# Performance work log

Measured on AMD Instinct MI355X. Metric: run time of the kernel, lower is better.

## Reference

```python
import jax, jax.numpy as jnp
import numpy as np

USER_COUNT = 100000
ITEM_COUNT = 50000
LATENT = 64
N_LAYERS = 3
NEG_SLOPE = 0.2


def _xavier(key, shape):
    fan_in, fan_out = shape[-2], shape[-1]
    lim = jnp.sqrt(6.0 / (fan_in + fan_out))
    return jax.random.uniform(key, shape, jnp.float32, -lim, lim)


def setup_inputs() -> dict:
    key = jax.random.key(0)
    ks = jax.random.split(key, 20)
    E = 2400000
    edge_index = jax.random.randint(ks[0], (2, E), 0, USER_COUNT + ITEM_COUNT, dtype=jnp.int64)
    user = jax.random.randint(ks[1], (4096,), 0, USER_COUNT, dtype=jnp.int64)
    item = jax.random.randint(ks[2], (4096,), 0, ITEM_COUNT, dtype=jnp.int64)
    inp = {"user": user, "item": item, "edge_index": edge_index}
    # online encoder params
    inp["user_emb_o"] = _xavier(ks[3], (USER_COUNT, LATENT))
    inp["item_emb_o"] = _xavier(ks[4], (ITEM_COUNT, LATENT))
    inp["W_o"] = _xavier(ks[5], (N_LAYERS, LATENT, LATENT))
    inp["att_src_o"] = _xavier(ks[6], (N_LAYERS, 1, LATENT))[:, 0, :]
    inp["att_dst_o"] = _xavier(ks[7], (N_LAYERS, 1, LATENT))[:, 0, :]
    inp["bias_o"] = jnp.zeros((N_LAYERS, LATENT), jnp.float32)
    # target encoder params (momentum copy; frozen in torch)
    inp["user_emb_t"] = _xavier(ks[8], (USER_COUNT, LATENT))
    inp["item_emb_t"] = _xavier(ks[9], (ITEM_COUNT, LATENT))
    inp["W_t"] = _xavier(ks[10], (N_LAYERS, LATENT, LATENT))
    inp["att_src_t"] = _xavier(ks[11], (N_LAYERS, 1, LATENT))[:, 0, :]
    inp["att_dst_t"] = _xavier(ks[12], (N_LAYERS, 1, LATENT))[:, 0, :]
    inp["bias_t"] = jnp.zeros((N_LAYERS, LATENT), jnp.float32)
    # predictor Linear(latent, latent)
    inp["pred_W"] = _xavier(ks[13], (LATENT, LATENT))
    inp["pred_b"] = jnp.zeros((LATENT,), jnp.float32)
    return inp


def _gat_conv(x, src, dst, n_nodes, W, a_src, a_dst, b):
    # PyG GATConv, heads=1, concat=True, add_self_loops handled by caller.
    h = x @ W                                   # [N, F]
    e = jax.nn.leaky_relu(jnp.take(h @ a_src, src) + jnp.take(h @ a_dst, dst), NEG_SLOPE)  # [E]
    m = jax.ops.segment_max(e, dst, num_segments=n_nodes)
    m = jnp.where(jnp.isfinite(m), m, 0.0)
    ex = jnp.exp(e - jnp.take(m, dst))
    den = jax.ops.segment_sum(ex, dst, num_segments=n_nodes)
    alpha = ex / jnp.take(den, dst)             # softmax over incoming edges per dst
    msg = alpha[:, None] * jnp.take(h, src, axis=0)  # [E, F]
    return jax.ops.segment_sum(msg, dst, num_segments=n_nodes) + b


def _encode(user_emb, item_emb, W, a_src, a_dst, bias, src, dst):
    x = jnp.concatenate([user_emb, item_emb], axis=0)  # [N, F]
    n_nodes = x.shape[0]
    for l in range(N_LAYERS):
        x = _gat_conv(x, src, dst, n_nodes, W[l], a_src[l], a_dst[l], bias[l])
    return x[:user_emb.shape[0]], x[user_emb.shape[0]:]


def reference(user_emb_o, item_emb_o, W_o, att_src_o, att_dst_o, bias_o,
              user_emb_t, item_emb_t, W_t, att_src_t, att_dst_t, bias_t,
              pred_W, pred_b, user, item, edge_index):
    n_nodes = user_emb_o.shape[0] + item_emb_o.shape[0]
    loops = jnp.arange(n_nodes, dtype=edge_index.dtype)
    src = jnp.concatenate([edge_index[0], loops])  # add self loops (PyG default)
    dst = jnp.concatenate([edge_index[1], loops])
    u_all_o, i_all_o = _encode(user_emb_o, item_emb_o, W_o, att_src_o, att_dst_o, bias_o, src, dst)
    u_all_t, i_all_t = _encode(user_emb_t, item_emb_t, W_t, att_src_t, att_dst_t, bias_t, src, dst)
    u_online = jnp.take(u_all_o, user, axis=0)
    i_online = jnp.take(i_all_o, item, axis=0)
    u_target = jnp.take(u_all_t, user, axis=0)
    i_target = jnp.take(i_all_t, item, axis=0)
    return (u_online @ pred_W.T + pred_b, u_target, i_online @ pred_W.T + pred_b, i_target)
```

## Files before the change

### kernel.cpp

```cpp
#include <hip/hip_runtime.h>
#include <math.h>
#include <stdint.h>

#define LAT 64
#define SLICE 16384
#define BIN_CHUNK 1024

static inline int cdiv(int a, int b) { return (a + b - 1) / b; }

__global__ void k_scan1(const int* __restrict__ cnt, int N, int* __restrict__ out, int* __restrict__ blk_sums) {
    __shared__ int sdata[256];
    int t = threadIdx.x, b = blockIdx.x;
    int base = b * 1024 + t * 4;
    int v[4];
    int s = 0;
#pragma unroll
    for (int u = 0; u < 4; u++) { int i = base + u; v[u] = (i < N) ? cnt[i] : 0; s += v[u]; }
    sdata[t] = s; __syncthreads();
    for (int off = 1; off < 256; off <<= 1) {
        int x = (t >= off) ? sdata[t - off] : 0;
        __syncthreads();
        sdata[t] += x;
        __syncthreads();
    }
    int run = sdata[t] - s;
#pragma unroll
    for (int u = 0; u < 4; u++) { int i = base + u; if (i < N) out[i] = run; run += v[u]; }
    if (t == 255) blk_sums[b] = sdata[255];
}

__global__ void k_scan2(int* __restrict__ blk_sums, int NB) {
    __shared__ int sdata[256];
    int t = threadIdx.x;
    int v = (t < NB) ? blk_sums[t] : 0;
    sdata[t] = v; __syncthreads();
    for (int off = 1; off < 256; off <<= 1) {
        int x = (t >= off) ? sdata[t - off] : 0;
        __syncthreads();
        sdata[t] += x;
        __syncthreads();
    }
    if (t < NB) blk_sums[t] = sdata[t] - v;
}

__global__ void k_scan3(int* __restrict__ row_ptr, const int* __restrict__ blk_offs, int N, int ET) {
    int t = threadIdx.x, b = blockIdx.x;
    int base = b * 1024 + t * 4;
    int off = blk_offs[b];
#pragma unroll
    for (int u = 0; u < 4; u++) { int i = base + u; if (i < N) row_ptr[i] += off; }
    if (b == 0 && t == 0) row_ptr[N] = ET;
}

__global__ __launch_bounds__(256) void k_binA(const int* __restrict__ src_arr, const int* __restrict__ dst_arr,
                                              int E, int N, int ET, int rsz, int bcap,
                                              int2* __restrict__ buckets, int* __restrict__ gcur,
                                              int* __restrict__ cnt) {
    __shared__ int lcnt[8], lbase[8];
    int t = threadIdx.x;
    for (int base = blockIdx.x * BIN_CHUNK; base < ET; base += gridDim.x * BIN_CHUNK) {
        if (t < 8) lcnt[t] = 0;
        __syncthreads();
        int s[4], d[4], r[4], lofs[4];
        int nval = 0;
        if (base + BIN_CHUNK <= E) {
            int4 s4 = ((const int4*)(src_arr + base))[t];
            int4 d4 = ((const int4*)(dst_arr + base))[t];
            s[0] = s4.x; s[1] = s4.y; s[2] = s4.z; s[3] = s4.w;
            d[0] = d4.x; d[1] = d4.y; d[2] = d4.z; d[3] = d4.w;
            nval = 4;
        } else {
            for (int k = 0; k < 4; k++) {
                int e = base + t * 4 + k;
                if (e < ET) {
                    if (e < E) { s[nval] = src_arr[e]; d[nval] = dst_arr[e]; }
                    else { s[nval] = e - E; d[nval] = e - E; }
                    nval++;
                }
            }
        }
        for (int k = 0; k < nval; k++) {
            r[k] = d[k] / rsz;
            lofs[k] = atomicAdd(&lcnt[r[k]], 1);
            atomicAdd(&cnt[d[k]], 1);
        }
        __syncthreads();
        if (t < 8) lbase[t] = atomicAdd(&gcur[t], lcnt[t]);
        __syncthreads();
        for (int k = 0; k < nval; k++) {
            buckets[(size_t)r[k] * bcap + lbase[r[k]] + lofs[k]] = make_int2(s[k], d[k]);
        }
        __syncthreads();
    }
}

__global__ __launch_bounds__(256) void k_binB(const int2* __restrict__ buckets, int bcap,
                                              const int* __restrict__ gcur,
                                              const int* __restrict__ row_ptr, int* __restrict__ cnt,
                                              int* __restrict__ csr_src) {
    int r = blockIdx.x & 7;
    int nb = blockIdx.x >> 3;
    int stride = (gridDim.x >> 3) * 256;
    int total = gcur[r];
    const int* bp = (const int*)(buckets + (size_t)r * bcap);
    for (int i = nb * 256 + threadIdx.x; i < total; i += stride) {
        int s = __builtin_nontemporal_load(bp + 2 * i);
        int d = __builtin_nontemporal_load(bp + 2 * i + 1);
        int pos = atomicAdd(&cnt[d], 1);
        csr_src[row_ptr[d] + pos] = s;
    }
}

__global__ void k_count(const int* __restrict__ dst_arr, int E, int N, int* __restrict__ cnt) {
    int e = blockIdx.x * blockDim.x + threadIdx.x;
    int ET = E + N;
    if (e < ET) {
        int d = (e < E) ? dst_arr[e] : (e - E);
        atomicAdd(&cnt[d], 1);
    }
}

__global__ void k_scatter(const int* __restrict__ src_arr, const int* __restrict__ dst_arr, int E, int N,
                          const int* __restrict__ row_ptr, int* __restrict__ cnt, int* __restrict__ csr_src) {
    int ET = E + N;
    int slice = blockIdx.x >> 3;
    int range = blockIdx.x & 7;
    int rsz = (N + 7) >> 3;
    int lo = range * rsz;
    int hi = lo + rsz; if (hi > N) hi = N;
    int base = slice * SLICE;
    int end = base + SLICE; if (end > ET) end = ET;
    for (int e = base + threadIdx.x; e < end; e += 256) {
        int s, d;
        if (e < E) { s = src_arr[e]; d = dst_arr[e]; }
        else { s = e - E; d = e - E; }
        if (d >= lo && d < hi) {
            int pos = atomicAdd(&cnt[d], 1);
            csr_src[row_ptr[d] + pos] = s;
        }
    }
}

__global__ __launch_bounds__(256) void k_gemm2m(const float* __restrict__ xo, const float* __restrict__ xt,
        const float* __restrict__ ueo, const float* __restrict__ ieo,
        const float* __restrict__ uet, const float* __restrict__ iet, int NU,
        const float* __restrict__ Wo, const float* __restrict__ Wt,
        const float* __restrict__ atso, const float* __restrict__ atdo,
        const float* __restrict__ atst, const float* __restrict__ atdt,
        float* __restrict__ h2, float* __restrict__ asp, float* __restrict__ adp, int N) {
    __shared__ float sW[64 * 64];
    __shared__ float sX[128 * 65];
    __shared__ float sAs[64], sAd[64];
    int enc = blockIdx.x & 1;
    int bb = blockIdx.x >> 1;
    const float* x = enc ? xt : xo;
    const float* ue = enc ? uet : ueo;
    const float* ie = enc ? iet : ieo;
    const float* W = enc ? Wt : Wo;
    const float* att_s = enc ? atst : atso;
    const float* att_d = enc ? atdt : atdo;
    float* h2e = h2 + enc * 64;
    int t = threadIdx.x;
    int row0 = bb * 128;
    {
        const float4* Wv = (const float4*)W;
        float4* sWv = (float4*)sW;
#pragma unroll
        for (int u = 0; u < 4; u++) sWv[t + 256 * u] = Wv[t + 256 * u];
    }
    if (t < 64) { sAs[t] = att_s[t]; sAd[t] = att_d[t]; }
    {
#pragma unroll
        for (int u = 0; u < 8; u++) {
            int idx = t + 256 * u;
            int r = idx >> 4, c4 = idx & 15;
            int grow = row0 + r;
            float4 v = make_float4(0.f, 0.f, 0.f, 0.f);
            if (grow < N) {
                const float* base = x ? (x + (size_t)grow * 64)
                                      : (grow < NU ? ue + (size_t)grow * 64 : ie + (size_t)(grow - NU) * 64);
                v = ((const float4*)base)[c4];
            }
            int cc = c4 * 4;
            sX[r * 65 + cc] = v.x; sX[r * 65 + cc + 1] = v.y; sX[r * 65 + cc + 2] = v.z; sX[r * 65 + cc + 3] = v.w;
        }
    }
    __syncthreads();
    int rl = t >> 2;
    int g = t & 3;
    int c0 = g * 16;
    int rA = rl * 2, rB = rA + 1;
    float accA[16], accB[16];
#pragma unroll
    for (int j = 0; j < 16; j++) { accA[j] = 0.f; accB[j] = 0.f; }
    for (int k = 0; k < 64; k++) {
        float xa = sX[rA * 65 + k];
        float xb = sX[rB * 65 + k];
        const float4* wr = (const float4*)&sW[k * 64 + c0];
        float4 w0 = wr[0], w1 = wr[1], w2 = wr[2], w3 = wr[3];
        accA[0] += xa * w0.x; accA[1] += xa * w0.y; accA[2] += xa * w0.z; accA[3] += xa * w0.w;
        accA[4] += xa * w1.x; accA[5] += xa * w1.y; accA[6] += xa * w1.z; accA[7] += xa * w1.w;
        accA[8] += xa * w2.x; accA[9] += xa * w2.y; accA[10] += xa * w2.z; accA[11] += xa * w2.w;
        accA[12] += xa * w3.x; accA[13] += xa * w3.y; accA[14] += xa * w3.z; accA[15] += xa * w3.w;
        accB[0] += xb * w0.x; accB[1] += xb * w0.y; accB[2] += xb * w0.z; accB[3] += xb * w0.w;
        accB[4] += xb * w1.x; accB[5] += xb * w1.y; accB[6] += xb * w1.z; accB[7] += xb * w1.w;
        accB[8] += xb * w2.x; accB[9] += xb * w2.y; accB[10] += xb * w2.z; accB[11] += xb * w2.w;
        accB[12] += xb * w3.x; accB[13] += xb * w3.y; accB[14] += xb * w3.z; accB[15] += xb * w3.w;
    }
    float sA = 0.f, dA = 0.f, sB = 0.f, dB = 0.f;
#pragma unroll
    for (int j = 0; j < 16; j++) {
        sA += accA[j] * sAs[c0 + j]; dA += accA[j] * sAd[c0 + j];
        sB += accB[j] * sAs[c0 + j]; dB += accB[j] * sAd[c0 + j];
    }
    sA += __shfl_xor(sA, 1); sA += __shfl_xor(sA, 2);
    dA += __shfl_xor(dA, 1); dA += __shfl_xor(dA, 2);
    sB += __shfl_xor(sB, 1); sB += __shfl_xor(sB, 2);
    dB += __shfl_xor(dB, 1); dB += __shfl_xor(dB, 2);
    int rowA = row0 + rA, rowB = row0 + rB;
    if (rowA < N) {
        if (g == 0) { asp[(size_t)rowA * 2 + enc] = sA; adp[(size_t)rowA * 2 + enc] = dA; }
        float4* hv = (float4*)&h2e[(size_t)rowA * 128 + c0];
        hv[0] = make_float4(accA[0], accA[1], accA[2], accA[3]);
        hv[1] = make_float4(accA[4], accA[5], accA[6], accA[7]);
        hv[2] = make_float4(accA[8], accA[9], accA[10], accA[11]);
        hv[3] = make_float4(accA[12], accA[13], accA[14], accA[15]);
    }
    if (rowB < N) {
        if (g == 0) { asp[(size_t)rowB * 2 + enc] = sB; adp[(size_t)rowB * 2 + enc] = dB; }
        float4* hv = (float4*)&h2e[(size_t)rowB * 128 + c0];
        hv[0] = make_float4(accB[0], accB[1], accB[2], accB[3]);
        hv[1] = make_float4(accB[4], accB[5], accB[6], accB[7]);
        hv[2] = make_float4(accB[8], accB[9], accB[10], accB[11]);
        hv[3] = make_float4(accB[12], accB[13], accB[14], accB[15]);
    }
}

__global__ __launch_bounds__(256) void k_agg2(const float* __restrict__ h2,
                                              const int* __restrict__ row_ptr, const int* __restrict__ csr_src,
                                              const float2* __restrict__ asv, const float2* __restrict__ adv,
                                              const float* __restrict__ bias_o, const float* __restrict__ bias_t,
                                              float* __restrict__ xo, float* __restrict__ xt, int N,
                                              const int* __restrict__ selu, const int* __restrict__ seli,
                                              int nSel, int nSelU, int NU,
                                              float* __restrict__ selxo, float* __restrict__ outT_u,
                                              float* __restrict__ outT_i) {
    int wid = threadIdx.x >> 6, lane = threadIdx.x & 63;
    int r = blockIdx.x * 4 + wid;
    int d;
    float *po, *pt;
    if (selu) {
        if (r >= nSel) return;
        if (r < nSelU) { d = selu[r]; pt = outT_u + (size_t)r * 64; }
        else { int rr = r - nSelU; d = seli[rr] + NU; pt = outT_i + (size_t)rr * 64; }
        po = selxo + (size_t)r * 64;
    } else {
        if (r >= N) return;
        d = r;
        po = xo + (size_t)d * 64;
        pt = xt + (size_t)d * 64;
    }
    int s0 = row_ptr[d], s1 = row_ptr[d + 1];
    float2 advv = adv[d];
    int j0 = s0 + lane;
    int sv0 = 0; float eo0 = -1e30f, et0 = -1e30f;
    if (j0 < s1) {
        sv0 = csr_src[j0];
        float2 a2 = asv[sv0];
        float eo = a2.x + advv.x; eo0 = (eo > 0.f) ? eo : 0.2f * eo;
        float et = a2.y + advv.y; et0 = (et > 0.f) ? et : 0.2f * et;
    }
    float mo = eo0, mt = et0;
    for (int j = j0 + 64; j < s1; j += 64) {
        float2 a2 = asv[csr_src[j]];
        float eo = a2.x + advv.x; eo = (eo > 0.f) ? eo : 0.2f * eo; mo = fmaxf(mo, eo);
        float et = a2.y + advv.y; et = (et > 0.f) ? et : 0.2f * et; mt = fmaxf(mt, et);
    }
#pragma unroll
    for (int o = 32; o; o >>= 1) { mo = fmaxf(mo, __shfl_xor(mo, o)); mt = fmaxf(mt, __shfl_xor(mt, o)); }
    float exo0 = (j0 < s1) ? expf(eo0 - mo) : 0.f;
    float ext0 = (j0 < s1) ? expf(et0 - mt) : 0.f;
    float so = exo0, st = ext0;
    for (int j = j0 + 64; j < s1; j += 64) {
        float2 a2 = asv[csr_src[j]];
        float eo = a2.x + advv.x; eo = (eo > 0.f) ? eo : 0.2f * eo; so += expf(eo - mo);
        float et = a2.y + advv.y; et = (et > 0.f) ? et : 0.2f * et; st += expf(et - mt);
    }
#pragma unroll
    for (int o = 32; o; o >>= 1) { so += __shfl_xor(so, o); st += __shfl_xor(st, o); }
    float invo = 1.f / so, invt = 1.f / st;
    exo0 *= invo; ext0 *= invt;
    int sub = lane >> 4, c4 = lane & 15;
    float4 ao = make_float4(0.f, 0.f, 0.f, 0.f);
    float4 at4 = make_float4(0.f, 0.f, 0.f, 0.f);
    for (int cb = s0; cb < s1; cb += 64) {
        int sv; float wo, wt;
        if (cb == s0) { sv = sv0; wo = exo0; wt = ext0; }
        else {
            int jj = cb + lane; sv = 0; wo = 0.f; wt = 0.f;
            if (jj < s1) {
                sv = csr_src[jj];
                float2 a2 = asv[sv];
                float eo = a2.x + advv.x; eo = (eo > 0.f) ? eo : 0.2f * eo; wo = expf(eo - mo) * invo;
                float et = a2.y + advv.y; et = (et > 0.f) ? et : 0.2f * et; wt = expf(et - mt) * invt;
            }
        }
        int c = s1 - cb; if (c > 64) c = 64;
        int q = 0;
        for (; q + 8 <= c; q += 8) {
            int ilA = q + sub, ilB = q + 4 + sub;
            int sA = __shfl(sv, ilA), sB = __shfl(sv, ilB);
            float oA = __shfl(wo, ilA), oB = __shfl(wo, ilB);
            float tA = __shfl(wt, ilA), tB = __shfl(wt, ilB);
            const float* ha = h2 + (size_t)sA * 128 + (c4 << 2);
            const float* hb = h2 + (size_t)sB * 128 + (c4 << 2);
            float4 hoA = *(const float4*)ha;
            float4 htA = *(const float4*)(ha + 64);
            float4 hoB = *(const float4*)hb;
            float4 htB = *(const float4*)(hb + 64);
            ao.x += oA * hoA.x; ao.y += oA * hoA.y; ao.z += oA * hoA.z; ao.w += oA * hoA.w;
            at4.x += tA * htA.x; at4.y += tA * htA.y; at4.z += tA * htA.z; at4.w += tA * htA.w;
            ao.x += oB * hoB.x; ao.y += oB * hoB.y; ao.z += oB * hoB.z; ao.w += oB * hoB.w;
            at4.x += tB * htB.x; at4.y += tB * htB.y; at4.z += tB * htB.z; at4.w += tB * htB.w;
        }
        for (; q < c; q += 4) {
            int il = q + sub;
            int s = __shfl(sv, il);
            float o_ = __shfl(wo, il);
            float t_ = __shfl(wt, il);
            const float* hb = h2 + (size_t)s * 128 + (c4 << 2);
            float4 ho = *(const float4*)hb;
            float4 ht = *(const float4*)(hb + 64);
            ao.x += o_ * ho.x; ao.y += o_ * ho.y; ao.z += o_ * ho.z; ao.w += o_ * ho.w;
            at4.x += t_ * ht.x; at4.y += t_ * ht.y; at4.z += t_ * ht.z; at4.w += t_ * ht.w;
        }
    }
#pragma unroll
    for (int o = 16; o <= 32; o <<= 1) {
        ao.x += __shfl_xor(ao.x, o); ao.y += __shfl_xor(ao.y, o);
        ao.z += __shfl_xor(ao.z, o); ao.w += __shfl_xor(ao.w, o);
        at4.x += __shfl_xor(at4.x, o); at4.y += __shfl_xor(at4.y, o);
        at4.z += __shfl_xor(at4.z, o); at4.w += __shfl_xor(at4.w, o);
    }
    if (lane < 16) {
        float4 bo = ((const float4*)bias_o)[c4];
        ao.x += bo.x; ao.y += bo.y; ao.z += bo.z; ao.w += bo.w;
        ((float4*)po)[c4] = ao;
        float4 bt = ((const float4*)bias_t)[c4];
        at4.x += bt.x; at4.y += bt.y; at4.z += bt.z; at4.w += bt.w;
        ((float4*)pt)[c4] = at4;
    }
}

__global__ __launch_bounds__(256) void k_gemm(const float* __restrict__ x,
                                              const float* __restrict__ ue, const float* __restrict__ ie, int NU,
                                              const float* __restrict__ W,
                                              const float* __restrict__ att_s, const float* __restrict__ att_d,
                                              float* __restrict__ h, float* __restrict__ as_, float* __restrict__ ad_,
                                              int N) {
    __shared__ float sW[64 * 64];
    __shared__ float sX[128 * 65];
    __shared__ float sAs[64], sAd[64];
    int t = threadIdx.x;
    int row0 = blockIdx.x * 128;
    {
        const float4* Wv = (const float4*)W;
        float4* sWv = (float4*)sW;
#pragma unroll
        for (int u = 0; u < 4; u++) sWv[t + 256 * u] = Wv[t + 256 * u];
    }
    if (t < 64) { sAs[t] = att_s[t]; sAd[t] = att_d[t]; }
    {
#pragma unroll
        for (int u = 0; u < 8; u++) {
            int idx = t + 256 * u;
            int r = idx >> 4, c4 = idx & 15;
            int grow = row0 + r;
            float4 v = make_float4(0.f, 0.f, 0.f, 0.f);
            if (grow < N) {
                const float* base = x ? (x + (size_t)grow * 64)
                                      : (grow < NU ? ue + (size_t)grow * 64 : ie + (size_t)(grow - NU) * 64);
                v = ((const float4*)base)[c4];
            }
            int cc = c4 * 4;
            sX[r * 65 + cc] = v.x; sX[r * 65 + cc + 1] = v.y; sX[r * 65 + cc + 2] = v.z; sX[r * 65 + cc + 3] = v.w;
        }
    }
    __syncthreads();
    int rl = t >> 2;
    int g = t & 3;
    int c0 = g * 16;
    int rA = rl * 2, rB = rA + 1;
    float accA[16], accB[16];
#pragma unroll
    for (int j = 0; j < 16; j++) { accA[j] = 0.f; accB[j] = 0.f; }
    for (int k = 0; k < 64; k++) {
        float xa = sX[rA * 65 + k];
        float xb = sX[rB * 65 + k];
        const float4* wr = (const float4*)&sW[k * 64 + c0];
        float4 w0 = wr[0], w1 = wr[1], w2 = wr[2], w3 = wr[3];
        accA[0] += xa * w0.x; accA[1] += xa * w0.y; accA[2] += xa * w0.z; accA[3] += xa * w0.w;
        accA[4] += xa * w1.x; accA[5] += xa * w1.y; accA[6] += xa * w1.z; accA[7] += xa * w1.w;
        accA[8] += xa * w2.x; accA[9] += xa * w2.y; accA[10] += xa * w2.z; accA[11] += xa * w2.w;
        accA[12] += xa * w3.x; accA[13] += xa * w3.y; accA[14] += xa * w3.z; accA[15] += xa * w3.w;
        accB[0] += xb * w0.x; accB[1] += xb * w0.y; accB[2] += xb * w0.z; accB[3] += xb * w0.w;
        accB[4] += xb * w1.x; accB[5] += xb * w1.y; accB[6] += xb * w1.z; accB[7] += xb * w1.w;
        accB[8] += xb * w2.x; accB[9] += xb * w2.y; accB[10] += xb * w2.z; accB[11] += xb * w2.w;
        accB[12] += xb * w3.x; accB[13] += xb * w3.y; accB[14] += xb * w3.z; accB[15] += xb * w3.w;
    }
    float sA = 0.f, dA = 0.f, sB = 0.f, dB = 0.f;
#pragma unroll
    for (int j = 0; j < 16; j++) {
        sA += accA[j] * sAs[c0 + j]; dA += accA[j] * sAd[c0 + j];
        sB += accB[j] * sAs[c0 + j]; dB += accB[j] * sAd[c0 + j];
    }
    sA += __shfl_xor(sA, 1); sA += __shfl_xor(sA, 2);
    dA += __shfl_xor(dA, 1); dA += __shfl_xor(dA, 2);
    sB += __shfl_xor(sB, 1); sB += __shfl_xor(sB, 2);
    dB += __shfl_xor(dB, 1); dB += __shfl_xor(dB, 2);
    int rowA = row0 + rA, rowB = row0 + rB;
    if (rowA < N) {
        if (g == 0) { as_[rowA] = sA; ad_[rowA] = dA; }
        float4* hv = (float4*)&h[(size_t)rowA * 64 + c0];
        hv[0] = make_float4(accA[0], accA[1], accA[2], accA[3]);
        hv[1] = make_float4(accA[4], accA[5], accA[6], accA[7]);
        hv[2] = make_float4(accA[8], accA[9], accA[10], accA[11]);
        hv[3] = make_float4(accA[12], accA[13], accA[14], accA[15]);
    }
    if (rowB < N) {
        if (g == 0) { as_[rowB] = sB; ad_[rowB] = dB; }
        float4* hv = (float4*)&h[(size_t)rowB * 64 + c0];
        hv[0] = make_float4(accB[0], accB[1], accB[2], accB[3]);
        hv[1] = make_float4(accB[4], accB[5], accB[6], accB[7]);
        hv[2] = make_float4(accB[8], accB[9], accB[10], accB[11]);
        hv[3] = make_float4(accB[12], accB[13], accB[14], accB[15]);
    }
}

__global__ __launch_bounds__(256) void k_agg(const float* __restrict__ h,
                                             const int* __restrict__ row_ptr, const int* __restrict__ csr_src,
                                             const float* __restrict__ as_, const float* __restrict__ ad_,
                                             const float* __restrict__ bias, float* __restrict__ xout, int N) {
    int wid = threadIdx.x >> 6, lane = threadIdx.x & 63;
    int d = blockIdx.x * 4 + wid;
    if (d >= N) return;
    int s0 = row_ptr[d], s1 = row_ptr[d + 1];
    float adv = ad_[d];
    int j0 = s0 + lane;
    int sv0 = 0; float ev0 = -1e30f;
    if (j0 < s1) {
        sv0 = csr_src[j0];
        float e = as_[sv0] + adv;
        ev0 = (e > 0.f) ? e : 0.2f * e;
    }
    float m = ev0;
    for (int j = j0 + 64; j < s1; j += 64) {
        float e = as_[csr_src[j]] + adv;
        e = (e > 0.f) ? e : 0.2f * e;
        m = fmaxf(m, e);
    }
#pragma unroll
    for (int o = 32; o; o >>= 1) m = fmaxf(m, __shfl_xor(m, o));
    float ex0 = (j0 < s1) ? expf(ev0 - m) : 0.f;
    float sum = ex0;
    for (int j = j0 + 64; j < s1; j += 64) {
        float e = as_[csr_src[j]] + adv;
        e = (e > 0.f) ? e : 0.2f * e;
        sum += expf(e - m);
    }
#pragma unroll
    for (int o = 32; o; o >>= 1) sum += __shfl_xor(sum, o);
    float inv = 1.f / sum;
    ex0 *= inv;
    int sub = lane >> 4;
    int c4 = lane & 15;
    float4 acc = make_float4(0.f, 0.f, 0.f, 0.f);
    for (int cbase = s0; cbase < s1; cbase += 64) {
        int sv; float ex;
        if (cbase == s0) { sv = sv0; ex = ex0; }
        else {
            int jj = cbase + lane;
            sv = 0; ex = 0.f;
            if (jj < s1) {
                sv = csr_src[jj];
                float e = as_[sv] + adv;
                e = (e > 0.f) ? e : 0.2f * e;
                ex = expf(e - m) * inv;
            }
        }
        int cnt2 = s1 - cbase; if (cnt2 > 64) cnt2 = 64;
        for (int q = 0; q < cnt2; q += 4) {
            int il = q + sub;
            float w = __shfl(ex, il);
            int s = __shfl(sv, il);
            const float4 hv = *(const float4*)&h[(size_t)s * 64 + (c4 << 2)];
            acc.x += w * hv.x; acc.y += w * hv.y; acc.z += w * hv.z; acc.w += w * hv.w;
        }
    }
#pragma unroll
    for (int o = 16; o <= 32; o <<= 1) {
        acc.x += __shfl_xor(acc.x, o);
        acc.y += __shfl_xor(acc.y, o);
        acc.z += __shfl_xor(acc.z, o);
        acc.w += __shfl_xor(acc.w, o);
    }
    if (lane < 16) {
        float4 bv = ((const float4*)bias)[c4];
        acc.x += bv.x; acc.y += bv.y; acc.z += bv.z; acc.w += bv.w;
        ((float4*)&xout[(size_t)d * 64])[c4] = acc;
    }
}

__global__ __launch_bounds__(256) void k_pred(const float* __restrict__ x, const int* __restrict__ idx,
                                              int nIdx, int rowOff, const float* __restrict__ W,
                                              const float* __restrict__ bvec, float* __restrict__ out) {
    __shared__ float sWt[64 * 65];
    int t = threadIdx.x;
#pragma unroll
    for (int u = 0; u < 16; u++) {
        int i = u * 256 + t;
        int c = i >> 6, k = i & 63;
        sWt[k * 65 + c] = W[i];
    }
    __syncthreads();
    int wid = t >> 6, lane = t & 63;
    int r = blockIdx.x * 4 + wid;
    if (r >= nIdx) return;
    int node = idx ? (idx[r] + rowOff) : (r + rowOff);
    float xr = x[(size_t)node * 64 + lane];
    float acc = bvec[lane];
    for (int k = 0; k < 64; k++)
        acc += __shfl(xr, k) * sWt[k * 65 + lane];
    out[(size_t)r * 64 + lane] = acc;
}

__global__ void k_gather(const float* __restrict__ x, const int* __restrict__ idx, int nIdx, int rowOff,
                         float* __restrict__ out) {
    int t = blockIdx.x * blockDim.x + threadIdx.x;
    if (t < nIdx * 64) {
        int r = t >> 6, c = t & 63;
        int node = idx[r] + rowOff;
        out[t] = x[(size_t)node * 64 + c];
    }
}

extern "C" void kernel_launch(void* const* d_in, const int* in_sizes, int n_in,
                              void* d_out, int out_size, void* d_ws, size_t ws_size,
                              hipStream_t stream) {
    const int* user = (const int*)d_in[0];
    const int* item = (const int*)d_in[1];
    const int* edge = (const int*)d_in[2];
    const float* user_emb_o = (const float*)d_in[3];
    const float* item_emb_o = (const float*)d_in[4];
    const float* W_o = (const float*)d_in[5];
    const float* att_src_o = (const float*)d_in[6];
    const float* att_dst_o = (const float*)d_in[7];
    const float* bias_o = (const float*)d_in[8];
    const float* user_emb_t = (const float*)d_in[9];
    const float* item_emb_t = (const float*)d_in[10];
    const float* W_t = (const float*)d_in[11];
    const float* att_src_t = (const float*)d_in[12];
    const float* att_dst_t = (const float*)d_in[13];
    const float* bias_t = (const float*)d_in[14];
    const float* pred_W = (const float*)d_in[15];
    const float* pred_b = (const float*)d_in[16];
    float* out = (float*)d_out;

    int E = in_sizes[2] / 2;
    int NU = in_sizes[3] / LAT;
    int NI = in_sizes[4] / LAT;
    int N = NU + NI;
    int ET = E + N;
    int nU = in_sizes[0];
    int nI = in_sizes[1];
    int nSel = nU + nI;
    int rsz = (N + 7) >> 3;

    const int* src_arr = edge;
    const int* dst_arr = edge + E;

    auto al = [](size_t v) { return (v + 255) & ~(size_t)255; };

    char* p = (char*)d_ws;
    float* x_o   = (float*)p;  p += al((size_t)N * LAT * 4);
    float* x_t   = (float*)p;  p += al((size_t)N * LAT * 4);
    float* h2    = (float*)p;  p += al((size_t)N * 2 * LAT * 4);
    float* asv   = (float*)p;  p += al((size_t)N * 8);
    float* adv   = (float*)p;  p += al((size_t)N * 8);
    int* row_ptr = (int*)p;    p += al((size_t)(N + 1) * 4);
    int* cnt     = (int*)p;    p += al((size_t)N * 4);
    int* csr_src = (int*)p;    p += al((size_t)ET * 4);
    int* blk     = (int*)p;    p += al(4096);
    int* gcur    = (int*)p;    p += al(64);
    float* xsel  = (float*)p;  p += al((size_t)nSel * LAT * 4);
    size_t need_primary = (size_t)(p - (char*)d_ws);

    int bcap = ET / 8 + 16384;
    int2* buckets = (int2*)x_o;

    bool primary = ws_size >= need_primary;

    if (primary) {
        hipMemsetAsync(cnt, 0, (size_t)N * 4, stream);
        hipMemsetAsync(gcur, 0, 32, stream);
        k_binA<<<1024, 256, 0, stream>>>(src_arr, dst_arr, E, N, ET, rsz, bcap, buckets, gcur, cnt);
        int NB = cdiv(N, 1024);
        k_scan1<<<NB, 256, 0, stream>>>(cnt, N, row_ptr, blk);
        k_scan2<<<1, 256, 0, stream>>>(blk, NB);
        k_scan3<<<NB, 256, 0, stream>>>(row_ptr, blk, N, ET);
        hipMemsetAsync(cnt, 0, (size_t)N * 4, stream);
        k_binB<<<1024, 256, 0, stream>>>(buckets, bcap, gcur, row_ptr, cnt, csr_src);

        for (int l = 0; l < 3; l++) {
            const float* xo_in = (l == 0) ? nullptr : x_o;
            const float* xt_in = (l == 0) ? nullptr : x_t;
            k_gemm2m<<<cdiv(N, 128) * 2, 256, 0, stream>>>(xo_in, xt_in,
                    user_emb_o, item_emb_o, user_emb_t, item_emb_t, NU,
                    W_o + l * 4096, W_t + l * 4096,
                    att_src_o + l * 64, att_dst_o + l * 64,
                    att_src_t + l * 64, att_dst_t + l * 64,
                    h2, asv, adv, N);
            if (l < 2) {
                k_agg2<<<cdiv(N, 4), 256, 0, stream>>>(h2, row_ptr, csr_src,
                        (const float2*)asv, (const float2*)adv,
                        bias_o + l * 64, bias_t + l * 64,
                        x_o, x_t, N,
                        nullptr, nullptr, 0, 0, NU, nullptr, nullptr, nullptr);
            } else {
                k_agg2<<<cdiv(nSel, 4), 256, 0, stream>>>(h2, row_ptr, csr_src,
                        (const float2*)asv, (const float2*)adv,
                        bias_o + l * 64, bias_t + l * 64,
                        nullptr, nullptr, N,
                        user, item, nSel, nU, NU,
                        xsel, out + (size_t)nU * LAT, out + (size_t)3 * nU * LAT);
            }
        }
        k_pred<<<cdiv(nU, 4), 256, 0, stream>>>(xsel, nullptr, nU, 0, pred_W, pred_b, out);
        k_pred<<<cdiv(nI, 4), 256, 0, stream>>>(xsel, nullptr, nI, nU, pred_W, pred_b,
                                                out + (size_t)2 * nU * LAT);
        return;
    }

    p = (char*)d_ws;
    float* x_cur = (float*)p;  p += al((size_t)N * LAT * 4);
    float* h     = (float*)p;  p += al((size_t)N * LAT * 4);
    float* as_   = (float*)p;  p += al((size_t)N * 4);
    float* ad_   = (float*)p;  p += al((size_t)N * 4);
    row_ptr = (int*)p;         p += al((size_t)(N + 1) * 4);
    cnt     = (int*)p;         p += al((size_t)N * 4);
    csr_src = (int*)p;         p += al((size_t)ET * 4);
    blk     = (int*)p;         p += al(4096);

    hipMemsetAsync(cnt, 0, (size_t)N * 4, stream);
    k_count<<<cdiv(ET, 256), 256, 0, stream>>>(dst_arr, E, N, cnt);
    int NB = cdiv(N, 1024);
    k_scan1<<<NB, 256, 0, stream>>>(cnt, N, row_ptr, blk);
    k_scan2<<<1, 256, 0, stream>>>(blk, NB);
    k_scan3<<<NB, 256, 0, stream>>>(row_ptr, blk, N, ET);
    hipMemsetAsync(cnt, 0, (size_t)N * 4, stream);
    k_scatter<<<cdiv(ET, SLICE) * 8, 256, 0, stream>>>(src_arr, dst_arr, E, N, row_ptr, cnt, csr_src);

    auto run_encoder = [&](const float* ue, const float* ie, const float* Wl,
                           const float* asl, const float* adl, const float* bl) {
        for (int l = 0; l < 3; l++) {
            const float* xin = (l == 0) ? nullptr : x_cur;
            k_gemm<<<cdiv(N, 128), 256, 0, stream>>>(xin, ue, ie, NU, Wl + l * 64 * 64, asl + l * 64,
                                                     adl + l * 64, h, as_, ad_, N);
            k_agg<<<cdiv(N, 4), 256, 0, stream>>>(h, row_ptr, csr_src, as_, ad_, bl + l * 64, x_cur, N);
        }
    };

    run_encoder(user_emb_o, item_emb_o, W_o, att_src_o, att_dst_o, bias_o);
    k_pred<<<cdiv(nU, 4), 256, 0, stream>>>(x_cur, user, nU, 0, pred_W, pred_b, out);
    k_pred<<<cdiv(nI, 4), 256, 0, stream>>>(x_cur, item, nI, NU, pred_W, pred_b, out + (size_t)2 * nU * LAT);

    run_encoder(user_emb_t, item_emb_t, W_t, att_src_t, att_dst_t, bias_t);
    k_gather<<<cdiv(nU * LAT, 256), 256, 0, stream>>>(x_cur, user, nU, 0, out + (size_t)nU * LAT);
    k_gather<<<cdiv(nI * LAT, 256), 256, 0, stream>>>(x_cur, item, nI, NU, out + (size_t)3 * nU * LAT);
}
```

Baseline: 847.5 us.

## Build CSR from binned buckets with implicit self-loops and countdown placement

Self-loop edges are no longer materialized in the bucket pass. The scan adds one per node and writes each node's self-loop into the first CSR slot. Degree counting moves from random atomics in the streaming bin pass to a separate pass over the destination-sorted buckets, which should improve atomic locality. The scatter pass counts down from the counts instead of re-zeroing them, which removes one memset, and gcur is zeroed in the same memset. The two predictor launches are merged into one, at the cost of an extra read pass over the buckets.

Measured after the change: 875.9 us. 1.03x slower.

```diff
diff --git a/kernel.cpp b/kernel.cpp
--- a/kernel.cpp
+++ b/kernel.cpp
@@ -15,7 +15,7 @@
     int v[4];
     int s = 0;
 #pragma unroll
-    for (int u = 0; u < 4; u++) { int i = base + u; v[u] = (i < N) ? cnt[i] : 0; s += v[u]; }
+    for (int u = 0; u < 4; u++) { int i = base + u; v[u] = (i < N) ? (cnt[i] + 1) : 0; s += v[u]; }
     sdata[t] = s; __syncthreads();
     for (int off = 1; off < 256; off <<= 1) {
         int x = (t >= off) ? sdata[t - off] : 0;
@@ -43,22 +43,29 @@
     if (t < NB) blk_sums[t] = sdata[t] - v;
 }
 
-__global__ void k_scan3(int* __restrict__ row_ptr, const int* __restrict__ blk_offs, int N, int ET) {
+__global__ void k_scan3(int* __restrict__ row_ptr, const int* __restrict__ blk_offs, int N, int ET,
+                        int* __restrict__ csr_src) {
     int t = threadIdx.x, b = blockIdx.x;
     int base = b * 1024 + t * 4;
     int off = blk_offs[b];
 #pragma unroll
-    for (int u = 0; u < 4; u++) { int i = base + u; if (i < N) row_ptr[i] += off; }
+    for (int u = 0; u < 4; u++) {
+        int i = base + u;
+        if (i < N) {
+            int fin = row_ptr[i] + off;
+            row_ptr[i] = fin;
+            csr_src[fin] = i;
+        }
+    }
     if (b == 0 && t == 0) row_ptr[N] = ET;
 }
 
 __global__ __launch_bounds__(256) void k_binA(const int* __restrict__ src_arr, const int* __restrict__ dst_arr,
-                                              int E, int N, int ET, int rsz, int bcap,
-                                              int2* __restrict__ buckets, int* __restrict__ gcur,
-                                              int* __restrict__ cnt) {
+                                              int E, int rsz, int bcap,
+                                              int2* __restrict__ buckets, int* __restrict__ gcur) {
     __shared__ int lcnt[8], lbase[8];
     int t = threadIdx.x;
-    for (int base = blockIdx.x * BIN_CHUNK; base < ET; base += gridDim.x * BIN_CHUNK) {
+    for (int base = blockIdx.x * BIN_CHUNK; base < E; base += gridDim.x * BIN_CHUNK) {
         if (t < 8) lcnt[t] = 0;
         __syncthreads();
         int s[4], d[4], r[4], lofs[4];
@@ -72,17 +79,12 @@
         } else {
             for (int k = 0; k < 4; k++) {
                 int e = base + t * 4 + k;
-                if (e < ET) {
-                    if (e < E) { s[nval] = src_arr[e]; d[nval] = dst_arr[e]; }
-                    else { s[nval] = e - E; d[nval] = e - E; }
-                    nval++;
-                }
+                if (e < E) { s[nval] = src_arr[e]; d[nval] = dst_arr[e]; nval++; }
             }
         }
         for (int k = 0; k < nval; k++) {
             r[k] = d[k] / rsz;
             lofs[k] = atomicAdd(&lcnt[r[k]], 1);
-            atomicAdd(&cnt[d[k]], 1);
         }
         __syncthreads();
         if (t < 8) lbase[t] = atomicAdd(&gcur[t], lcnt[t]);
@@ -91,6 +93,19 @@
             buckets[(size_t)r[k] * bcap + lbase[r[k]] + lofs[k]] = make_int2(s[k], d[k]);
         }
         __syncthreads();
+    }
+}
+
+__global__ __launch_bounds__(256) void k_binCnt(const int2* __restrict__ buckets, int bcap,
+                                                const int* __restrict__ gcur, int* __restrict__ cnt) {
+    int r = blockIdx.x & 7;
+    int nb = blockIdx.x >> 3;
+    int stride = (gridDim.x >> 3) * 256;
+    int total = gcur[r];
+    const int* bp = (const int*)(buckets + (size_t)r * bcap);
+    for (int i = nb * 256 + threadIdx.x; i < total; i += stride) {
+        int d = __builtin_nontemporal_load(bp + 2 * i + 1);
+        atomicAdd(&cnt[d], 1);
     }
 }
 
@@ -106,7 +121,7 @@
     for (int i = nb * 256 + threadIdx.x; i < total; i += stride) {
         int s = __builtin_nontemporal_load(bp + 2 * i);
         int d = __builtin_nontemporal_load(bp + 2 * i + 1);
-        int pos = atomicAdd(&cnt[d], 1);
+        int pos = atomicSub(&cnt[d], 1);
         csr_src[row_ptr[d] + pos] = s;
     }
 }
@@ -118,6 +133,36 @@
         int d = (e < E) ? dst_arr[e] : (e - E);
         atomicAdd(&cnt[d], 1);
     }
+}
+
+__global__ void k_scan3f(int* __restrict__ row_ptr, const int* __restrict__ blk_offs, int N, int ET) {
+    int t = threadIdx.x, b = blockIdx.x;
+    int base = b * 1024 + t * 4;
+    int off = blk_offs[b];
+#pragma unroll
+    for (int u = 0; u < 4; u++) { int i = base + u; if (i < N) row_ptr[i] += off; }
+    if (b == 0 && t == 0) row_ptr[N] = ET;
+}
+
+__global__ void k_scan1f(const int* __restrict__ cnt, int N, int* __restrict__ out, int* __restrict__ blk_sums) {
+    __shared__ int sdata[256];
+    int t = threadIdx.x, b = blockIdx.x;
+    int base = b * 1024 + t * 4;
+    int v[4];
+    int s = 0;
+#pragma unroll
+    for (int u = 0; u < 4; u++) { int i = base + u; v[u] = (i < N) ? cnt[i] : 0; s += v[u]; }
+    sdata[t] = s; __syncthreads();
+    for (int off = 1; off < 256; off <<= 1) {
+        int x = (t >= off) ? sdata[t - off] : 0;
+        __syncthreads();
+        sdata[t] += x;
+        __syncthreads();
+    }
+    int run = sdata[t] - s;
+#pragma unroll
+    for (int u = 0; u < 4; u++) { int i = base + u; if (i < N) out[i] = run; run += v[u]; }
+    if (t == 255) blk_sums[b] = sdata[255];
 }
 
 __global__ void k_scatter(const int* __restrict__ src_arr, const int* __restrict__ dst_arr, int E, int N,
@@ -511,6 +556,29 @@
     }
 }
 
+__global__ __launch_bounds__(256) void k_pred2(const float* __restrict__ x, int nU, int nI,
+                                               const float* __restrict__ W, const float* __restrict__ bvec,
+                                               float* __restrict__ outU, float* __restrict__ outI) {
+    __shared__ float sWt[64 * 65];
+    int t = threadIdx.x;
+#pragma unroll
+    for (int u = 0; u < 16; u++) {
+        int i = u * 256 + t;
+        int c = i >> 6, k = i & 63;
+        sWt[k * 65 + c] = W[i];
+    }
+    __syncthreads();
+    int wid = t >> 6, lane = t & 63;
+    int r = blockIdx.x * 4 + wid;
+    if (r >= nU + nI) return;
+    float xr = x[(size_t)r * 64 + lane];
+    float acc = bvec[lane];
+    for (int k = 0; k < 64; k++)
+        acc += __shfl(xr, k) * sWt[k * 65 + lane];
+    float* dst = (r < nU) ? (outU + (size_t)r * 64) : (outI + (size_t)(r - nU) * 64);
+    dst[lane] = acc;
+}
+
 __global__ __launch_bounds__(256) void k_pred(const float* __restrict__ x, const int* __restrict__ idx,
                                               int nIdx, int rowOff, const float* __restrict__ W,
                                               const float* __restrict__ bvec, float* __restrict__ out) {
@@ -588,27 +656,26 @@
     float* asv   = (float*)p;  p += al((size_t)N * 8);
     float* adv   = (float*)p;  p += al((size_t)N * 8);
     int* row_ptr = (int*)p;    p += al((size_t)(N + 1) * 4);
-    int* cnt     = (int*)p;    p += al((size_t)N * 4);
+    int* cnt     = (int*)p;    size_t cntsz = al((size_t)N * 4); p += cntsz;
+    int* gcur    = (int*)p;    p += al(64);
     int* csr_src = (int*)p;    p += al((size_t)ET * 4);
     int* blk     = (int*)p;    p += al(4096);
-    int* gcur    = (int*)p;    p += al(64);
     float* xsel  = (float*)p;  p += al((size_t)nSel * LAT * 4);
     size_t need_primary = (size_t)(p - (char*)d_ws);
 
-    int bcap = ET / 8 + 16384;
+    int bcap = E / 8 + 16384;
     int2* buckets = (int2*)x_o;
 
     bool primary = ws_size >= need_primary;
 
     if (primary) {
-        hipMemsetAsync(cnt, 0, (size_t)N * 4, stream);
-        hipMemsetAsync(gcur, 0, 32, stream);
-        k_binA<<<1024, 256, 0, stream>>>(src_arr, dst_arr, E, N, ET, rsz, bcap, buckets, gcur, cnt);
+        hipMemsetAsync(cnt, 0, cntsz + 64, stream);
+        k_binA<<<1024, 256, 0, stream>>>(src_arr, dst_arr, E, rsz, bcap, buckets, gcur);
+        k_binCnt<<<128, 256, 0, stream>>>(buckets, bcap, gcur, cnt);
         int NB = cdiv(N, 1024);
         k_scan1<<<NB, 256, 0, stream>>>(cnt, N, row_ptr, blk);
         k_scan2<<<1, 256, 0, stream>>>(blk, NB);
-        k_scan3<<<NB, 256, 0, stream>>>(row_ptr, blk, N, ET);
-        hipMemsetAsync(cnt, 0, (size_t)N * 4, stream);
+        k_scan3<<<NB, 256, 0, stream>>>(row_ptr, blk, N, ET, csr_src);
         k_binB<<<1024, 256, 0, stream>>>(buckets, bcap, gcur, row_ptr, cnt, csr_src);
 
         for (int l = 0; l < 3; l++) {
@@ -635,9 +702,8 @@
                         xsel, out + (size_t)nU * LAT, out + (size_t)3 * nU * LAT);
             }
         }
-        k_pred<<<cdiv(nU, 4), 256, 0, stream>>>(xsel, nullptr, nU, 0, pred_W, pred_b, out);
-        k_pred<<<cdiv(nI, 4), 256, 0, stream>>>(xsel, nullptr, nI, nU, pred_W, pred_b,
-                                                out + (size_t)2 * nU * LAT);
+        k_pred2<<<cdiv(nSel, 4), 256, 0, stream>>>(xsel, nU, nI, pred_W, pred_b,
+                                                   out, out + (size_t)2 * nU * LAT);
         return;
     }
 
@@ -654,9 +720,9 @@
     hipMemsetAsync(cnt, 0, (size_t)N * 4, stream);
     k_count<<<cdiv(ET, 256), 256, 0, stream>>>(dst_arr, E, N, cnt);
     int NB = cdiv(N, 1024);
-    k_scan1<<<NB, 256, 0, stream>>>(cnt, N, row_ptr, blk);
+    k_scan1f<<<NB, 256, 0, stream>>>(cnt, N, row_ptr, blk);
     k_scan2<<<1, 256, 0, stream>>>(blk, NB);
-    k_scan3<<<NB, 256, 0, stream>>>(row_ptr, blk, N, ET);
+    k_scan3f<<<NB, 256, 0, stream>>>(row_ptr, blk, N, ET);
     hipMemsetAsync(cnt, 0, (size_t)N * 4, stream);
     k_scatter<<<cdiv(ET, SLICE) * 8, 256, 0, stream>>>(src_arr, dst_arr, E, N, row_ptr, cnt, csr_src);
 
```

## Fuse layer-0 GEMM with edge binning in one launch and merge predictor kernels

Applied to the files above, without the earlier changes.

Adds a combined kernel in which the first blocks run the layer-0 GEMM straight from the user and item embeddings, and the remaining blocks run the edge-binning pass. The two independent stages can therefore overlap on the GPU. The two memsets are merged into one by placing gcur right after cnt, and the two predictor launches become a single kernel covering users and items. The cost is that binning blocks now reserve the GEMM's large shared-memory footprint, which may lower their occupancy.

Measured after the change: 837.2 us, median of 2. About the same (-1.2%).

```diff
diff --git a/kernel.cpp b/kernel.cpp
--- a/kernel.cpp
+++ b/kernel.cpp
@@ -52,45 +52,142 @@
     if (b == 0 && t == 0) row_ptr[N] = ET;
 }
 
-__global__ __launch_bounds__(256) void k_binA(const int* __restrict__ src_arr, const int* __restrict__ dst_arr,
-                                              int E, int N, int ET, int rsz, int bcap,
-                                              int2* __restrict__ buckets, int* __restrict__ gcur,
-                                              int* __restrict__ cnt) {
-    __shared__ int lcnt[8], lbase[8];
+__global__ __launch_bounds__(256) void k_l0(
+        const float* __restrict__ ueo, const float* __restrict__ ieo,
+        const float* __restrict__ uet, const float* __restrict__ iet, int NU,
+        const float* __restrict__ Wo, const float* __restrict__ Wt,
+        const float* __restrict__ atso, const float* __restrict__ atdo,
+        const float* __restrict__ atst, const float* __restrict__ atdt,
+        float* __restrict__ h2, float* __restrict__ asp, float* __restrict__ adp, int N,
+        int gemmGrid, int binGrid,
+        const int* __restrict__ src_arr, const int* __restrict__ dst_arr,
+        int E, int ET, int rsz, int bcap,
+        int2* __restrict__ buckets, int* __restrict__ gcur, int* __restrict__ cnt) {
+    __shared__ float sW[64 * 64];
+    __shared__ float sX[128 * 65];
+    __shared__ float sAs[64], sAd[64];
     int t = threadIdx.x;
-    for (int base = blockIdx.x * BIN_CHUNK; base < ET; base += gridDim.x * BIN_CHUNK) {
-        if (t < 8) lcnt[t] = 0;
-        __syncthreads();
-        int s[4], d[4], r[4], lofs[4];
-        int nval = 0;
-        if (base + BIN_CHUNK <= E) {
-            int4 s4 = ((const int4*)(src_arr + base))[t];
-            int4 d4 = ((const int4*)(dst_arr + base))[t];
-            s[0] = s4.x; s[1] = s4.y; s[2] = s4.z; s[3] = s4.w;
-            d[0] = d4.x; d[1] = d4.y; d[2] = d4.z; d[3] = d4.w;
-            nval = 4;
-        } else {
-            for (int k = 0; k < 4; k++) {
-                int e = base + t * 4 + k;
-                if (e < ET) {
-                    if (e < E) { s[nval] = src_arr[e]; d[nval] = dst_arr[e]; }
-                    else { s[nval] = e - E; d[nval] = e - E; }
-                    nval++;
+
+    if ((int)blockIdx.x >= gemmGrid) {
+        int* lcnt = (int*)sW;
+        int* lbase = (int*)sW + 8;
+        int bb = blockIdx.x - gemmGrid;
+        for (int base = bb * BIN_CHUNK; base < ET; base += binGrid * BIN_CHUNK) {
+            if (t < 8) lcnt[t] = 0;
+            __syncthreads();
+            int s[4], d[4], r[4], lofs[4];
+            int nval = 0;
+            if (base + BIN_CHUNK <= E) {
+                int4 s4 = ((const int4*)(src_arr + base))[t];
+                int4 d4 = ((const int4*)(dst_arr + base))[t];
+                s[0] = s4.x; s[1] = s4.y; s[2] = s4.z; s[3] = s4.w;
+                d[0] = d4.x; d[1] = d4.y; d[2] = d4.z; d[3] = d4.w;
+                nval = 4;
+            } else {
+                for (int k = 0; k < 4; k++) {
+                    int e = base + t * 4 + k;
+                    if (e < ET) {
+                        if (e < E) { s[nval] = src_arr[e]; d[nval] = dst_arr[e]; }
+                        else { s[nval] = e - E; d[nval] = e - E; }
+                        nval++;
+                    }
                 }
             }
-        }
-        for (int k = 0; k < nval; k++) {
-            r[k] = d[k] / rsz;
-            lofs[k] = atomicAdd(&lcnt[r[k]], 1);
-            atomicAdd(&cnt[d[k]], 1);
-        }
-        __syncthreads();
-        if (t < 8) lbase[t] = atomicAdd(&gcur[t], lcnt[t]);
-        __syncthreads();
-        for (int k = 0; k < nval; k++) {
-            buckets[(size_t)r[k] * bcap + lbase[r[k]] + lofs[k]] = make_int2(s[k], d[k]);
-        }
-        __syncthreads();
+            for (int k = 0; k < nval; k++) {
+                r[k] = d[k] / rsz;
+                lofs[k] = atomicAdd(&lcnt[r[k]], 1);
+                atomicAdd(&cnt[d[k]], 1);
+            }
+            __syncthreads();
+            if (t < 8) lbase[t] = atomicAdd(&gcur[t], lcnt[t]);
+            __syncthreads();
+            for (int k = 0; k < nval; k++) {
+                buckets[(size_t)r[k] * bcap + lbase[r[k]] + lofs[k]] = make_int2(s[k], d[k]);
+            }
+            __syncthreads();
+        }
+        return;
+    }
+
+    int enc = blockIdx.x & 1;
+    int bb = blockIdx.x >> 1;
+    const float* ue = enc ? uet : ueo;
+    const float* ie = enc ? iet : ieo;
+    const float* W = enc ? Wt : Wo;
+    const float* att_s = enc ? atst : atso;
+    const float* att_d = enc ? atdt : atdo;
+    float* h2e = h2 + enc * 64;
+    int row0 = bb * 128;
+    {
+        const float4* Wv = (const float4*)W;
+        float4* sWv = (float4*)sW;
+#pragma unroll
+        for (int u = 0; u < 4; u++) sWv[t + 256 * u] = Wv[t + 256 * u];
+    }
+    if (t < 64) { sAs[t] = att_s[t]; sAd[t] = att_d[t]; }
+    {
+#pragma unroll
+        for (int u = 0; u < 8; u++) {
+            int idx = t + 256 * u;
+            int r = idx >> 4, c4 = idx & 15;
+            int grow = row0 + r;
+            float4 v = make_float4(0.f, 0.f, 0.f, 0.f);
+            if (grow < N) {
+                const float* base = (grow < NU) ? ue + (size_t)grow * 64 : ie + (size_t)(grow - NU) * 64;
+                v = ((const float4*)base)[c4];
+            }
+            int cc = c4 * 4;
+            sX[r * 65 + cc] = v.x; sX[r * 65 + cc + 1] = v.y; sX[r * 65 + cc + 2] = v.z; sX[r * 65 + cc + 3] = v.w;
+        }
+    }
+    __syncthreads();
+    int rl = t >> 2;
+    int g = t & 3;
+    int c0 = g * 16;
+    int rA = rl * 2, rB = rA + 1;
+    float accA[16], accB[16];
+#pragma unroll
+    for (int j = 0; j < 16; j++) { accA[j] = 0.f; accB[j] = 0.f; }
+    for (int k = 0; k < 64; k++) {
+        float xa = sX[rA * 65 + k];
+        float xb = sX[rB * 65 + k];
+        const float4* wr = (const float4*)&sW[k * 64 + c0];
+        float4 w0 = wr[0], w1 = wr[1], w2 = wr[2], w3 = wr[3];
+        accA[0] += xa * w0.x; accA[1] += xa * w0.y; accA[2] += xa * w0.z; accA[3] += xa * w0.w;
+        accA[4] += xa * w1.x; accA[5] += xa * w1.y; accA[6] += xa * w1.z; accA[7] += xa * w1.w;
+        accA[8] += xa * w2.x; accA[9] += xa * w2.y; accA[10] += xa * w2.z; accA[11] += xa * w2.w;
+        accA[12] += xa * w3.x; accA[13] += xa * w3.y; accA[14] += xa * w3.z; accA[15] += xa * w3.w;
+        accB[0] += xb * w0.x; accB[1] += xb * w0.y; accB[2] += xb * w0.z; accB[3] += xb * w0.w;
+        accB[4] += xb * w1.x; accB[5] += xb * w1.y; accB[6] += xb * w1.z; accB[7] += xb * w1.w;
+        accB[8] += xb * w2.x; accB[9] += xb * w2.y; accB[10] += xb * w2.z; accB[11] += xb * w2.w;
+        accB[12] += xb * w3.x; accB[13] += xb * w3.y; accB[14] += xb * w3.z; accB[15] += xb * w3.w;
+    }
+    float sA = 0.f, dA = 0.f, sB = 0.f, dB = 0.f;
+#pragma unroll
+    for (int j = 0; j < 16; j++) {
+        sA += accA[j] * sAs[c0 + j]; dA += accA[j] * sAd[c0 + j];
+        sB += accB[j] * sAs[c0 + j]; dB += accB[j] * sAd[c0 + j];
+    }
+    sA += __shfl_xor(sA, 1); sA += __shfl_xor(sA, 2);
+    dA += __shfl_xor(dA, 1); dA += __shfl_xor(dA, 2);
+    sB += __shfl_xor(sB, 1); sB += __shfl_xor(sB, 2);
+    dB += __shfl_xor(dB, 1); dB += __shfl_xor(dB, 2);
+    int rowA = row0 + rA, rowB = row0 + rB;
+    if (rowA < N) {
+        if (g == 0) { asp[(size_t)rowA * 2 + enc] = sA; adp[(size_t)rowA * 2 + enc] = dA; }
+        float4* hv = (float4*)&h2e[(size_t)rowA * 128 + c0];
+        hv[0] = make_float4(accA[0], accA[1], accA[2], accA[3]);
+        hv[1] = make_float4(accA[4], accA[5], accA[6], accA[7]);
+        hv[2] = make_float4(accA[8], accA[9], accA[10], accA[11]);
+        hv[3] = make_float4(accA[12], accA[13], accA[14], accA[15]);
+    }
+    if (rowB < N) {
+        if (g == 0) { asp[(size_t)rowB * 2 + enc] = sB; adp[(size_t)rowB * 2 + enc] = dB; }
+        float4* hv = (float4*)&h2e[(size_t)rowB * 128 + c0];
+        hv[0] = make_float4(accB[0], accB[1], accB[2], accB[3]);
+        hv[1] = make_float4(accB[4], accB[5], accB[6], accB[7]);
+        hv[2] = make_float4(accB[8], accB[9], accB[10], accB[11]);
+        hv[3] = make_float4(accB[12], accB[13], accB[14], accB[15]);
     }
 }
 
@@ -111,39 +208,8 @@
     }
 }
 
-__global__ void k_count(const int* __restrict__ dst_arr, int E, int N, int* __restrict__ cnt) {
-    int e = blockIdx.x * blockDim.x + threadIdx.x;
-    int ET = E + N;
-    if (e < ET) {
-        int d = (e < E) ? dst_arr[e] : (e - E);
-        atomicAdd(&cnt[d], 1);
-    }
-}
-
-__global__ void k_scatter(const int* __restrict__ src_arr, const int* __restrict__ dst_arr, int E, int N,
-                          const int* __restrict__ row_ptr, int* __restrict__ cnt, int* __restrict__ csr_src) {
-    int ET = E + N;
-    int slice = blockIdx.x >> 3;
-    int range = blockIdx.x & 7;
-    int rsz = (N + 7) >> 3;
-    int lo = range * rsz;
-    int hi = lo + rsz; if (hi > N) hi = N;
-    int base = slice * SLICE;
-    int end = base + SLICE; if (end > ET) end = ET;
-    for (int e = base + threadIdx.x; e < end; e += 256) {
-        int s, d;
-        if (e < E) { s = src_arr[e]; d = dst_arr[e]; }
-        else { s = e - E; d = e - E; }
-        if (d >= lo && d < hi) {
-            int pos = atomicAdd(&cnt[d], 1);
-            csr_src[row_ptr[d] + pos] = s;
-        }
-    }
-}
-
 __global__ __launch_bounds__(256) void k_gemm2m(const float* __restrict__ xo, const float* __restrict__ xt,
-        const float* __restrict__ ueo, const float* __restrict__ ieo,
-        const float* __restrict__ uet, const float* __restrict__ iet, int NU,
+        int NU,
         const float* __restrict__ Wo, const float* __restrict__ Wt,
         const float* __restrict__ atso, const float* __restrict__ atdo,
         const float* __restrict__ atst, const float* __restrict__ atdt,
@@ -154,8 +220,6 @@
     int enc = blockIdx.x & 1;
     int bb = blockIdx.x >> 1;
     const float* x = enc ? xt : xo;
-    const float* ue = enc ? uet : ueo;
-    const float* ie = enc ? iet : ieo;
     const float* W = enc ? Wt : Wo;
     const float* att_s = enc ? atst : atso;
     const float* att_d = enc ? atdt : atdo;
@@ -176,11 +240,7 @@
             int r = idx >> 4, c4 = idx & 15;
             int grow = row0 + r;
             float4 v = make_float4(0.f, 0.f, 0.f, 0.f);
-            if (grow < N) {
-                const float* base = x ? (x + (size_t)grow * 64)
-                                      : (grow < NU ? ue + (size_t)grow * 64 : ie + (size_t)(grow - NU) * 64);
-                v = ((const float4*)base)[c4];
-            }
+            if (grow < N) v = ((const float4*)(x + (size_t)grow * 64))[c4];
             int cc = c4 * 4;
             sX[r * 65 + cc] = v.x; sX[r * 65 + cc + 1] = v.y; sX[r * 65 + cc + 2] = v.z; sX[r * 65 + cc + 3] = v.w;
         }
@@ -352,6 +412,59 @@
     }
 }
 
+__global__ __launch_bounds__(256) void k_pred2(const float* __restrict__ x, int nU, int nI,
+                                               const float* __restrict__ W, const float* __restrict__ bvec,
+                                               float* __restrict__ outU, float* __restrict__ outI) {
+    __shared__ float sWt[64 * 65];
+    int t = threadIdx.x;
+#pragma unroll
+    for (int u = 0; u < 16; u++) {
+        int i = u * 256 + t;
+        int c = i >> 6, k = i & 63;
+        sWt[k * 65 + c] = W[i];
+    }
+    __syncthreads();
+    int wid = t >> 6, lane = t & 63;
+    int r = blockIdx.x * 4 + wid;
+    if (r >= nU + nI) return;
+    float xr = x[(size_t)r * 64 + lane];
+    float acc = bvec[lane];
+    for (int k = 0; k < 64; k++)
+        acc += __shfl(xr, k) * sWt[k * 65 + lane];
+    float* dst = (r < nU) ? (outU + (size_t)r * 64) : (outI + (size_t)(r - nU) * 64);
+    dst[lane] = acc;
+}
+
+__global__ void k_count(const int* __restrict__ dst_arr, int E, int N, int* __restrict__ cnt) {
+    int e = blockIdx.x * blockDim.x + threadIdx.x;
+    int ET = E + N;
+    if (e < ET) {
+        int d = (e < E) ? dst_arr[e] : (e - E);
+        atomicAdd(&cnt[d], 1);
+    }
+}
+
+__global__ void k_scatter(const int* __restrict__ src_arr, const int* __restrict__ dst_arr, int E, int N,
+                          const int* __restrict__ row_ptr, int* __restrict__ cnt, int* __restrict__ csr_src) {
+    int ET = E + N;
+    int slice = blockIdx.x >> 3;
+    int range = blockIdx.x & 7;
+    int rsz = (N + 7) >> 3;
+    int lo = range * rsz;
+    int hi = lo + rsz; if (hi > N) hi = N;
+    int base = slice * SLICE;
+    int end = base + SLICE; if (end > ET) end = ET;
+    for (int e = base + threadIdx.x; e < end; e += 256) {
+        int s, d;
+        if (e < E) { s = src_arr[e]; d = dst_arr[e]; }
+        else { s = e - E; d = e - E; }
+        if (d >= lo && d < hi) {
+            int pos = atomicAdd(&cnt[d], 1);
+            csr_src[row_ptr[d] + pos] = s;
+        }
+    }
+}
+
 __global__ __launch_bounds__(256) void k_gemm(const float* __restrict__ x,
                                               const float* __restrict__ ue, const float* __restrict__ ie, int NU,
                                               const float* __restrict__ W,
@@ -588,10 +701,10 @@
     float* asv   = (float*)p;  p += al((size_t)N * 8);
     float* adv   = (float*)p;  p += al((size_t)N * 8);
     int* row_ptr = (int*)p;    p += al((size_t)(N + 1) * 4);
-    int* cnt     = (int*)p;    p += al((size_t)N * 4);
+    int* cnt     = (int*)p;    size_t cntsz = al((size_t)N * 4); p += cntsz;
+    int* gcur    = (int*)p;    p += al(64);
     int* csr_src = (int*)p;    p += al((size_t)ET * 4);
     int* blk     = (int*)p;    p += al(4096);
-    int* gcur    = (int*)p;    p += al(64);
     float* xsel  = (float*)p;  p += al((size_t)nSel * LAT * 4);
     size_t need_primary = (size_t)(p - (char*)d_ws);
 
@@ -601,9 +714,16 @@
     bool primary = ws_size >= need_primary;
 
     if (primary) {
-        hipMemsetAsync(cnt, 0, (size_t)N * 4, stream);
-        hipMemsetAsync(gcur, 0, 32, stream);
-        k_binA<<<1024, 256, 0, stream>>>(src_arr, dst_arr, E, N, ET, rsz, bcap, buckets, gcur, cnt);
+        int gemmGrid = cdiv(N, 128) * 2;
+        int binGrid = 1024;
+        hipMemsetAsync(cnt, 0, cntsz + 64, stream);
+        k_l0<<<gemmGrid + binGrid, 256, 0, stream>>>(
+                user_emb_o, item_emb_o, user_emb_t, item_emb_t, NU,
+                W_o, W_t, att_src_o, att_dst_o, att_src_t, att_dst_t,
+                h2, asv, adv, N,
+                gemmGrid, binGrid,
+                src_arr, dst_arr, E, ET, rsz, bcap,
+                buckets, gcur, cnt);
         int NB = cdiv(N, 1024);
         k_scan1<<<NB, 256, 0, stream>>>(cnt, N, row_ptr, blk);
         k_scan2<<<1, 256, 0, stream>>>(blk, NB);
@@ -612,14 +732,13 @@
         k_binB<<<1024, 256, 0, stream>>>(buckets, bcap, gcur, row_ptr, cnt, csr_src);
 
         for (int l = 0; l < 3; l++) {
-            const float* xo_in = (l == 0) ? nullptr : x_o;
-            const float* xt_in = (l == 0) ? nullptr : x_t;
-            k_gemm2m<<<cdiv(N, 128) * 2, 256, 0, stream>>>(xo_in, xt_in,
-                    user_emb_o, item_emb_o, user_emb_t, item_emb_t, NU,
-                    W_o + l * 4096, W_t + l * 4096,
-                    att_src_o + l * 64, att_dst_o + l * 64,
-                    att_src_t + l * 64, att_dst_t + l * 64,
-                    h2, asv, adv, N);
+            if (l > 0) {
+                k_gemm2m<<<cdiv(N, 128) * 2, 256, 0, stream>>>(x_o, x_t, NU,
+                        W_o + l * 4096, W_t + l * 4096,
+                        att_src_o + l * 64, att_dst_o + l * 64,
+                        att_src_t + l * 64, att_dst_t + l * 64,
+                        h2, asv, adv, N);
+            }
             if (l < 2) {
                 k_agg2<<<cdiv(N, 4), 256, 0, stream>>>(h2, row_ptr, csr_src,
                         (const float2*)asv, (const float2*)adv,
@@ -635,9 +754,8 @@
                         xsel, out + (size_t)nU * LAT, out + (size_t)3 * nU * LAT);
             }
         }
-        k_pred<<<cdiv(nU, 4), 256, 0, stream>>>(xsel, nullptr, nU, 0, pred_W, pred_b, out);
-        k_pred<<<cdiv(nI, 4), 256, 0, stream>>>(xsel, nullptr, nI, nU, pred_W, pred_b,
-                                                out + (size_t)2 * nU * LAT);
+        k_pred2<<<cdiv(nSel, 4), 256, 0, stream>>>(xsel, nU, nI, pred_W, pred_b,
+                                                   out, out + (size_t)2 * nU * LAT);
         return;
     }
 
```
